# Performance work log

Measured on AMD Instinct MI355X. Metric: run time of the kernel, lower is better.

The kernel has to match this reference:

```python
import jax, jax.numpy as jnp
import numpy as np

B, H, W, CIN, COUT = 4, 128, 128, 16, 16
FH, FW = 2 * H - 1, 2 * W - 1  # fft_shape = 2*k - 1 per spatial dim (SAME, stride 1)


def setup_inputs() -> dict:
    key = jax.random.key(0)
    k1, k2, k3, k4 = jax.random.split(key, 4)
    inputs = jax.random.normal(k1, (B, H, W, CIN), dtype=jnp.float32)
    # Fourier-space complex kernel, represented as two real arrays
    kernel_real = jax.random.normal(k2, (FH, FW, CIN, COUT), dtype=jnp.float32) * 0.05
    kernel_imag = jax.random.normal(k3, (FH, FW, CIN, COUT), dtype=jnp.float32) * 0.05
    bias = jax.random.normal(k4, (1, 1, 1, COUT), dtype=jnp.float32) * 0.01
    return {"inputs": inputs, "kernel_real": kernel_real, "kernel_imag": kernel_imag, "bias": bias}


def reference(inputs, kernel_real, kernel_imag, bias):
    kernel = kernel_real + 1j * kernel_imag  # (FH, FW, CIN, COUT) complex64
    b, h, w, cin = inputs.shape
    fft_shape = (2 * h - 1, 2 * w - 1)
    # FFT over spatial dims, zero-padded to fft_shape -> (B, FH, FW, CIN) complex64
    y = jnp.fft.fftn(inputs, axes=(1, 2), s=fft_shape)
    # Broadcast complex multiply + inverse FFT: (B, FH, FW, CIN, COUT)
    y = jnp.fft.ifftn(y[..., None] * kernel, axes=(1, 2)).real
    # 'SAME' slice: center crop back to the input spatial size
    sh = (fft_shape[0] - h) // 2
    sw = (fft_shape[1] - w) // 2
    y = y[:, sh:sh + h, sw:sw + w]  # (B, H, W, CIN, COUT)
    # Faithful to the source: sum over axis=-1 (the `features` axis), leaving CIN channels
    y = jnp.sum(y, axis=-1)  # (B, H, W, CIN)
    return y + bias  # bias broadcasts because COUT == CIN
```

## Files before the change

kernel.cpp:

```cpp
#include <hip/hip_runtime.h>
#include <math.h>


constexpr float PI2_OVER_N = 6.28318530717958647692f / 255.0f;
constexpr float INV_N2 = 1.0f / (255.0f * 255.0f);

typedef __attribute__((ext_vector_type(8))) short bf16x8;
typedef __attribute__((ext_vector_type(4))) float f32x4;
#define MFMA16 __builtin_amdgcn_mfma_f32_16x16x32_bf16

__device__ __forceinline__ int remap_bc(int xidx) {
  int k = xidx & 7, j = xidx >> 3;
  return ((k >> 1) * 16) + ((k & 1) * 8) + j;
}

__device__ __forceinline__ unsigned short bf16h(float f) {
  unsigned u = __float_as_uint(f);
  return (unsigned short)((u + 0x7FFFu + ((u >> 16) & 1u)) >> 16);
}
__device__ __forceinline__ float bf16f(unsigned short h) {
  return __uint_as_float(((unsigned)h) << 16);
}


__device__ __forceinline__ void ksum_body(
    int buf, int xb, const float* __restrict__ kr, const float* __restrict__ ki,
    float* __restrict__ Sr, float* __restrict__ Si) {
  const int nrows = 255 * 255 * 16;
  int r = xb * 256 + threadIdx.x;
  if (r >= nrows) return;
  const float* src = (buf == 0) ? kr : ki;
  float* dst = (buf == 0) ? Sr : Si;
  const float4* k4 = (const float4*)(src + (size_t)r * 16);
  float4 a = k4[0], b = k4[1], c = k4[2], d = k4[3];
  dst[r] = a.x + a.y + a.z + a.w + b.x + b.y + b.z + b.w +
           c.x + c.y + c.z + c.w + d.x + d.y + d.z + d.w;
}

__device__ __forceinline__ void packx_body(
    int pid, const float* __restrict__ x, short* __restrict__ xp) {
  int bc = pid & 63;
  int mt = pid >> 6;
  int b = bc >> 4, c = bc & 15;
  int mcol = threadIdx.x & 15;
  int noct = threadIdx.x >> 4;
  int m = mt * 16 + mcol;
  const float* xs = x + ((size_t)(b * 128 + m) * 128 + noct * 8) * 16 + c;
  unsigned short hi[8], lo[8];
#pragma unroll
  for (int j = 0; j < 8; ++j) {
    float v = xs[j * 16];
    hi[j] = bf16h(v);
    lo[j] = bf16h(v - bf16f(hi[j]));
  }
  size_t base = (size_t)bc * 32768 + ((size_t)(mt * 16 + noct) * 16 + mcol) * 8;
  uint4 o;
  o.x = (unsigned)hi[0] | ((unsigned)hi[1] << 16);
  o.y = (unsigned)hi[2] | ((unsigned)hi[3] << 16);
  o.z = (unsigned)hi[4] | ((unsigned)hi[5] << 16);
  o.w = (unsigned)hi[6] | ((unsigned)hi[7] << 16);
  *(uint4*)(xp + base) = o;
  o.x = (unsigned)lo[0] | ((unsigned)lo[1] << 16);
  o.y = (unsigned)lo[2] | ((unsigned)lo[3] << 16);
  o.z = (unsigned)lo[4] | ((unsigned)lo[5] << 16);
  o.w = (unsigned)lo[6] | ((unsigned)lo[7] << 16);
  *(uint4*)(xp + base + 16384) = o;
}

__device__ __forceinline__ void buildt1_body(int cid, short* __restrict__ t1) {
  int i = cid * 256 + threadIdx.x;
  int plane = i >> 14;
  int r = i & 16383;
  int qt = r >> 11, noct = (r >> 7) & 15, qcol = (r >> 3) & 15, j = r & 7;
  int q = qt * 16 + qcol, n = noct * 8 + j;
  float s, c;
  sincosf(PI2_OVER_N * (float)((q * n) % 255), &s, &c);
  float src = (plane < 2) ? c : -s;
  unsigned short hh = bf16h(src);
  t1[i] = (short)((plane & 1) ? bf16h(src - bf16f(hh)) : hh);
}

__device__ __forceinline__ void buildt24_body(
    int cid2, short* __restrict__ t2, short* __restrict__ t4, short* __restrict__ t5) {
  int i = cid2 * 256 + threadIdx.x;
  float s, c;
  if (i < 196608) {
    int plane = i >> 15;
    int r = i & 32767;
    int pt = r >> 11, r2 = r & 2047;
    int moct = r2 >> 7, p = (r2 >> 3) & 15, j = r2 & 7;
    int pg = pt * 16 + p, m = moct * 8 + j;
    int k = ((pg % 255) * m) % 255;
    sincosf(PI2_OVER_N * (float)k, &s, &c);
    float ti = -s;
    float src = (plane < 2) ? c : ((plane < 4) ? ti : -ti);
    unsigned short h = bf16h(src);
    t2[i] = (short)((plane & 1) ? bf16h(src - bf16f(h)) : h);
  } else if (i < 393216) {
    int i2 = i - 196608;
    int plane = i2 >> 15;
    int r = i2 & 32767;
    int ht = r >> 12, r2 = r & 4095;
    int poct = r2 >> 7, h = (r2 >> 3) & 15, j = r2 & 7;
    int p = poct * 8 + j;
    unsigned short val = 0;
    if (p < 255) {
      int hg = ht * 16 + h;
      int k = ((hg + 63) * p) % 255;
      sincosf(PI2_OVER_N * (float)k, &s, &c);
      float src = (plane < 2) ? c : ((plane < 4) ? s : -s);
      unsigned short hh = bf16h(src);
      val = (plane & 1) ? bf16h(src - bf16f(hh)) : hh;
    }
    t4[i2] = (short)val;
  } else {
    int i3 = i - 393216;
    int plane = i3 >> 15;
    int r = i3 & 32767;
    int wt = r >> 12, r2 = r & 4095;
    int ko = r2 >> 7, wl = (r2 >> 3) & 15, j = r2 & 7;
    int q = (ko * 8 + j) & 127;
    int ww = wt * 16 + wl;
    sincosf(PI2_OVER_N * (float)(((ww + 63) * q) % 255), &s, &c);
    float src = (plane < 2) ? c : -s;
    unsigned short hh = bf16h(src);
    t5[i3] = (short)((plane & 1) ? bf16h(src - bf16f(hh)) : hh);
  }
}

__global__ __launch_bounds__(256) void fused_front(
    const float* __restrict__ kr, const float* __restrict__ ki,
    float* __restrict__ Sr, float* __restrict__ Si,
    const float* __restrict__ x, short* __restrict__ xp,
    short* __restrict__ t1, short* __restrict__ t2,
    short* __restrict__ t4, short* __restrict__ t5) {
  int bid = blockIdx.x;
  int d = bid >> 2, r = bid & 3;
  if (r == 3) {
    if (d < 512)      packx_body(d, x, xp);
    else if (d < 768) buildt1_body(d - 512, t1);
    else              buildt24_body(d - 768, t2, t4, t5);
  } else {
    int kid = d * 3 + r;
    if (kid < 8192) ksum_body(kid & 1, kid >> 1, kr, ki, Sr, Si);
  }
}


__device__ __forceinline__ void fold_body(
    int fid, const float* __restrict__ Sr, const float* __restrict__ Si,
    float2* __restrict__ keff2) {
  int p = fid % 255;
  int qy = fid / 255;
  int q = qy * 16 + (threadIdx.x >> 4);
  int c = threadIdx.x & 15;
  int pp = (255 - p) % 255;
  int qq = (255 - q) % 255;
  size_t i0 = (size_t)(p * 255 + q) * 16 + c;
  size_t i1 = (size_t)(pp * 255 + qq) * 16 + c;
  float sr0 = Sr[i0], si0 = Si[i0], sr1 = Sr[i1], si1 = Si[i1];
  float2 v;
  v.x = 0.5f * (sr0 + sr1);
  v.y = 0.5f * (si0 - si1);
  keff2[((size_t)c * 255 + p) * 128 + q] = v;
}

__device__ __forceinline__ void s1g_body(
    int gid, const short* __restrict__ xp, const short* __restrict__ t1,
    short* __restrict__ ub) {
  int bc = gid & 63;
  int mt = gid >> 6;
  int w = threadIdx.x >> 6;
  int lane = threadIdx.x & 63;
  int quad = lane >> 4, col = lane & 15;
  f32x4 ur[2] = {{0,0,0,0},{0,0,0,0}};
  f32x4 ui[2] = {{0,0,0,0},{0,0,0,0}};
  const short* xb = xp + (size_t)bc * 32768;
#pragma unroll
  for (int ko = 0; ko < 4; ++ko) {
    int noct = ko * 4 + quad;
    const short* pa = xb + ((size_t)(mt * 16 + noct) * 16 + col) * 8;
    bf16x8 xh = *(const bf16x8*)(pa);
    bf16x8 xl = *(const bf16x8*)(pa + 16384);
#pragma unroll
    for (int qq = 0; qq < 2; ++qq) {
      int qt = w * 2 + qq;
      const short* pb = t1 + ((size_t)(qt * 16 + noct) * 16 + col) * 8;
      bf16x8 ch = *(const bf16x8*)(pb);
      bf16x8 cl = *(const bf16x8*)(pb + 16384);
      bf16x8 nh = *(const bf16x8*)(pb + 2 * 16384);
      bf16x8 nl = *(const bf16x8*)(pb + 3 * 16384);
      ur[qq] = MFMA16(xh, ch, ur[qq], 0, 0, 0);
      ur[qq] = MFMA16(xh, cl, ur[qq], 0, 0, 0);
      ur[qq] = MFMA16(xl, ch, ur[qq], 0, 0, 0);
      ur[qq] = MFMA16(xl, cl, ur[qq], 0, 0, 0);
      ui[qq] = MFMA16(xh, nh, ui[qq], 0, 0, 0);
      ui[qq] = MFMA16(xh, nl, ui[qq], 0, 0, 0);
      ui[qq] = MFMA16(xl, nh, ui[qq], 0, 0, 0);
      ui[qq] = MFMA16(xl, nl, ui[qq], 0, 0, 0);
    }
  }
  int moct = mt * 2 + (quad >> 1);
  int j0 = (quad & 1) * 4;
#pragma unroll
  for (int qq = 0; qq < 2; ++qq) {
    int qt = w * 2 + qq;
    unsigned short rh[4], rl[4], ih[4], il[4];
#pragma unroll
    for (int r = 0; r < 4; ++r) {
      rh[r] = bf16h(ur[qq][r]); rl[r] = bf16h(ur[qq][r] - bf16f(rh[r]));
      ih[r] = bf16h(ui[qq][r]); il[r] = bf16h(ui[qq][r] - bf16f(ih[r]));
    }
    size_t base = (size_t)bc * 65536 + (size_t)qt * 2048 + (size_t)moct * 128 +
                  (size_t)col * 8 + j0;
    uint2 o;
    o.x = (unsigned)rh[0] | ((unsigned)rh[1] << 16);
    o.y = (unsigned)rh[2] | ((unsigned)rh[3] << 16);
    *(uint2*)(ub + base) = o;
    o.x = (unsigned)rl[0] | ((unsigned)rl[1] << 16);
    o.y = (unsigned)rl[2] | ((unsigned)rl[3] << 16);
    *(uint2*)(ub + base + 16384) = o;
    o.x = (unsigned)ih[0] | ((unsigned)ih[1] << 16);
    o.y = (unsigned)ih[2] | ((unsigned)ih[3] << 16);
    *(uint2*)(ub + base + 2 * 16384) = o;
    o.x = (unsigned)il[0] | ((unsigned)il[1] << 16);
    o.y = (unsigned)il[2] | ((unsigned)il[3] << 16);
    *(uint2*)(ub + base + 3 * 16384) = o;
  }
}

__global__ __launch_bounds__(256) void mid(
    const float* __restrict__ Sr, const float* __restrict__ Si,
    float2* __restrict__ keff2,
    const short* __restrict__ xp, const short* __restrict__ t1,
    short* __restrict__ ub) {
  int bid = blockIdx.x;
  int d = bid / 5, r = bid - d * 5;
  if (r == 4) {
    s1g_body(d, xp, t1, ub);
  } else {
    int fid = d * 4 + r;
    if (fid < 2040) fold_body(fid, Sr, Si, keff2);
  }
}

__global__ __launch_bounds__(256) void stage2_mfma(
    const short* __restrict__ ub, const short* __restrict__ t2,
    const float2* __restrict__ keff2, short* __restrict__ zb) {
  int bc = remap_bc(blockIdx.x);
  int c = bc & 15;
  int w = threadIdx.x >> 6;
  int lane = threadIdx.x & 63;
  int quad = lane >> 4, col = lane & 15;
  int pt0 = blockIdx.y * 2;
  int qh = w;
  f32x4 accr[2][2] = {{{0,0,0,0},{0,0,0,0}},{{0,0,0,0},{0,0,0,0}}};
  f32x4 acci[2][2] = {{{0,0,0,0},{0,0,0,0}},{{0,0,0,0},{0,0,0,0}}};
  const short* ubase = ub + (size_t)bc * 65536;
#pragma unroll
  for (int ko = 0; ko < 4; ++ko) {
    int moct = ko * 4 + quad;
    bf16x8 brh[2], brl[2], bih[2], bil[2];
#pragma unroll
    for (int qq = 0; qq < 2; ++qq) {
      int qt = qh * 2 + qq;
      const short* tb = ubase + ((size_t)(qt * 16 + moct) * 16 + col) * 8;
      brh[qq] = *(const bf16x8*)(tb);
      brl[qq] = *(const bf16x8*)(tb + 16384);
      bih[qq] = *(const bf16x8*)(tb + 2 * 16384);
      bil[qq] = *(const bf16x8*)(tb + 3 * 16384);
    }
#pragma unroll
    for (int ptl = 0; ptl < 2; ++ptl) {
      int pt = pt0 + ptl;
      const short* ta = t2 + ((size_t)(pt * 16 + moct) * 16 + col) * 8;
      bf16x8 arh = *(const bf16x8*)(ta);
      bf16x8 arl = *(const bf16x8*)(ta + 32768);
      bf16x8 aih = *(const bf16x8*)(ta + 2 * 32768);
      bf16x8 ail = *(const bf16x8*)(ta + 3 * 32768);
      bf16x8 anh = *(const bf16x8*)(ta + 4 * 32768);
      bf16x8 anl = *(const bf16x8*)(ta + 5 * 32768);
#pragma unroll
      for (int qq = 0; qq < 2; ++qq) {
        accr[ptl][qq] = MFMA16(arh, brh[qq], accr[ptl][qq], 0, 0, 0);
        accr[ptl][qq] = MFMA16(arh, brl[qq], accr[ptl][qq], 0, 0, 0);
        accr[ptl][qq] = MFMA16(arl, brh[qq], accr[ptl][qq], 0, 0, 0);
        accr[ptl][qq] = MFMA16(anh, bih[qq], accr[ptl][qq], 0, 0, 0);
        accr[ptl][qq] = MFMA16(anh, bil[qq], accr[ptl][qq], 0, 0, 0);
        accr[ptl][qq] = MFMA16(anl, bih[qq], accr[ptl][qq], 0, 0, 0);
        acci[ptl][qq] = MFMA16(arh, bih[qq], acci[ptl][qq], 0, 0, 0);
        acci[ptl][qq] = MFMA16(arh, bil[qq], acci[ptl][qq], 0, 0, 0);
        acci[ptl][qq] = MFMA16(arl, bih[qq], acci[ptl][qq], 0, 0, 0);
        acci[ptl][qq] = MFMA16(aih, brh[qq], acci[ptl][qq], 0, 0, 0);
        acci[ptl][qq] = MFMA16(aih, brl[qq], acci[ptl][qq], 0, 0, 0);
        acci[ptl][qq] = MFMA16(ail, brh[qq], acci[ptl][qq], 0, 0, 0);
      }
    }
  }
  size_t joff = (size_t)col * 8 + (quad & 1) * 4;
#pragma unroll
  for (int ptl = 0; ptl < 2; ++ptl) {
    int pt = pt0 + ptl;
    int poct = pt * 2 + (quad >> 1);
#pragma unroll
    for (int qq = 0; qq < 2; ++qq) {
      int qt = qh * 2 + qq;
      int qg = qt * 16 + col;
      float zr[4], zi[4];
#pragma unroll
      for (int r = 0; r < 4; ++r) {
        int pg = pt * 16 + quad * 4 + r;
        int pgc = pg < 255 ? pg : 254;
        float2 k = keff2[((size_t)c * 255 + pgc) * 128 + qg];
        float xr = accr[ptl][qq][r], xi = acci[ptl][qq][r];
        zr[r] = k.x * xr - k.y * xi;
        zi[r] = k.x * xi + k.y * xr;
      }
      unsigned short hr[4], lr[4], hi_[4], li[4];
#pragma unroll
      for (int r = 0; r < 4; ++r) {
        hr[r] = bf16h(zr[r]);  lr[r] = bf16h(zr[r] - bf16f(hr[r]));
        hi_[r] = bf16h(zi[r]); li[r] = bf16h(zi[r] - bf16f(hi_[r]));
      }
      size_t base = (size_t)bc * 131072 + (size_t)qt * 4096 + (size_t)poct * 128 + joff;
      uint2 o;
      o.x = (unsigned)hr[0] | ((unsigned)hr[1] << 16);
      o.y = (unsigned)hr[2] | ((unsigned)hr[3] << 16);
      *(uint2*)(zb + base) = o;
      o.x = (unsigned)lr[0] | ((unsigned)lr[1] << 16);
      o.y = (unsigned)lr[2] | ((unsigned)lr[3] << 16);
      *(uint2*)(zb + base + 32768) = o;
      o.x = (unsigned)hi_[0] | ((unsigned)hi_[1] << 16);
      o.y = (unsigned)hi_[2] | ((unsigned)hi_[3] << 16);
      *(uint2*)(zb + base + 2 * 32768) = o;
      o.x = (unsigned)li[0] | ((unsigned)li[1] << 16);
      o.y = (unsigned)li[2] | ((unsigned)li[3] << 16);
      *(uint2*)(zb + base + 3 * 32768) = o;
    }
  }
}

__global__ __launch_bounds__(256) void stage4_mfma(
    const short* __restrict__ zb, const short* __restrict__ t4,
    short* __restrict__ a5, float* __restrict__ v0) {
  int bc = remap_bc(blockIdx.x);
  int w = threadIdx.x >> 6;
  int lane = threadIdx.x & 63;
  int quad = lane >> 4, col = lane & 15;
  int u = blockIdx.y * 4 + w;
  int qt = u >> 3;
  int kseg = (u >> 2) & 1;
  int htp = u & 3;
  f32x4 accr[2] = {{0,0,0,0},{0,0,0,0}};
  f32x4 acci[2] = {{0,0,0,0},{0,0,0,0}};
  const short* zbase = zb + (size_t)bc * 131072;
#pragma unroll
  for (int ko = 0; ko < 4; ++ko) {
    int poct = kseg * 16 + ko * 4 + quad;
    const short* tz = zbase + ((size_t)(qt * 32 + poct) * 16 + col) * 8;
    bf16x8 zrh = *(const bf16x8*)(tz);
    bf16x8 zrl = *(const bf16x8*)(tz + 32768);
    bf16x8 zih = *(const bf16x8*)(tz + 2 * 32768);
    bf16x8 zil = *(const bf16x8*)(tz + 3 * 32768);
#pragma unroll
    for (int t = 0; t < 2; ++t) {
      int ht = htp * 2 + t;
      const short* ta = t4 + ((size_t)(ht * 32 + poct) * 16 + col) * 8;
      bf16x8 trh = *(const bf16x8*)(ta);
      bf16x8 trl = *(const bf16x8*)(ta + 32768);
      bf16x8 tih = *(const bf16x8*)(ta + 2 * 32768);
      bf16x8 til = *(const bf16x8*)(ta + 3 * 32768);
      bf16x8 tnh = *(const bf16x8*)(ta + 4 * 32768);
      bf16x8 tnl = *(const bf16x8*)(ta + 5 * 32768);
      accr[t] = MFMA16(zrh, trh, accr[t], 0, 0, 0);
      accr[t] = MFMA16(zrh, trl, accr[t], 0, 0, 0);
      accr[t] = MFMA16(zrl, trh, accr[t], 0, 0, 0);
      accr[t] = MFMA16(zih, tnh, accr[t], 0, 0, 0);
      accr[t] = MFMA16(zih, tnl, accr[t], 0, 0, 0);
      accr[t] = MFMA16(zil, tnh, accr[t], 0, 0, 0);
      acci[t] = MFMA16(zih, trh, acci[t], 0, 0, 0);
      acci[t] = MFMA16(zih, trl, acci[t], 0, 0, 0);
      acci[t] = MFMA16(zil, trh, acci[t], 0, 0, 0);
      acci[t] = MFMA16(zrh, tih, acci[t], 0, 0, 0);
      acci[t] = MFMA16(zrh, til, acci[t], 0, 0, 0);
      acci[t] = MFMA16(zrl, tih, acci[t], 0, 0, 0);
    }
  }
  int ko_s = kseg * 16 + qt * 2 + (quad >> 1);
  int j0 = (quad & 1) * 4;
#pragma unroll
  for (int t = 0; t < 2; ++t) {
    int ht = htp * 2 + t;
    unsigned short vh[4], vl[4], wh[4], wl2[4];
#pragma unroll
    for (int r = 0; r < 4; ++r) {
      vh[r] = bf16h(accr[t][r]);  vl[r] = bf16h(accr[t][r] - bf16f(vh[r]));
      wh[r] = bf16h(acci[t][r]);  wl2[r] = bf16h(acci[t][r] - bf16f(wh[r]));
    }
    size_t base = (((size_t)(bc * 4) * 8 + ht) * 32 + ko_s) * 128 + (size_t)col * 8 + j0;
    uint2 o;
    o.x = (unsigned)vh[0] | ((unsigned)vh[1] << 16);
    o.y = (unsigned)vh[2] | ((unsigned)vh[3] << 16);
    *(uint2*)(a5 + base) = o;
    o.x = (unsigned)vl[0] | ((unsigned)vl[1] << 16);
    o.y = (unsigned)vl[2] | ((unsigned)vl[3] << 16);
    *(uint2*)(a5 + base + 32768) = o;
    o.x = (unsigned)wh[0] | ((unsigned)wh[1] << 16);
    o.y = (unsigned)wh[2] | ((unsigned)wh[3] << 16);
    *(uint2*)(a5 + base + 2 * 32768) = o;
    o.x = (unsigned)wl2[0] | ((unsigned)wl2[1] << 16);
    o.y = (unsigned)wl2[2] | ((unsigned)wl2[3] << 16);
    *(uint2*)(a5 + base + 3 * 32768) = o;
    if (qt == 0 && quad == 0)
      v0[(size_t)(kseg * 64 + bc) * 128 + ht * 16 + col] = accr[t][0];
  }
}

__global__ __launch_bounds__(256) void stage5_mfma(
    const short* __restrict__ a5, const short* __restrict__ t5,
    const float* __restrict__ v0, const float* __restrict__ bias,
    float* __restrict__ out) {
  int bc = remap_bc(blockIdx.x);
  int w = threadIdx.x >> 6;
  int lane = threadIdx.x & 63;
  int quad = lane >> 4, col = lane & 15;
  int u = blockIdx.y * 4 + w;
  int ht = u >> 2;
  int wtp = u & 3;
  f32x4 acc[2] = {{0,0,0,0},{0,0,0,0}};
  const short* abase = a5 + (size_t)bc * 131072;
#pragma unroll
  for (int kc = 0; kc < 8; ++kc) {
    int koq = kc * 4 + quad;
    const short* pa = abase + ((size_t)(ht * 32 + koq) * 16 + col) * 8;
    bf16x8 vrh = *(const bf16x8*)(pa);
    bf16x8 vrl = *(const bf16x8*)(pa + 32768);
    bf16x8 vih = *(const bf16x8*)(pa + 2 * 32768);
    bf16x8 vil = *(const bf16x8*)(pa + 3 * 32768);
#pragma unroll
    for (int t = 0; t < 2; ++t) {
      int wt = wtp * 2 + t;
      const short* pb = t5 + ((size_t)(wt * 32 + koq) * 16 + col) * 8;
      bf16x8 tch = *(const bf16x8*)(pb);
      bf16x8 tcl = *(const bf16x8*)(pb + 32768);
      bf16x8 tnh = *(const bf16x8*)(pb + 2 * 32768);
      bf16x8 tnl = *(const bf16x8*)(pb + 3 * 32768);
      acc[t] = MFMA16(vrh, tch, acc[t], 0, 0, 0);
      acc[t] = MFMA16(vrh, tcl, acc[t], 0, 0, 0);
      acc[t] = MFMA16(vrl, tch, acc[t], 0, 0, 0);
      acc[t] = MFMA16(vih, tnh, acc[t], 0, 0, 0);
      acc[t] = MFMA16(vih, tnl, acc[t], 0, 0, 0);
      acc[t] = MFMA16(vil, tnh, acc[t], 0, 0, 0);
    }
  }
  int b = bc >> 4, c = bc & 15;
  float bb = bias[c];
  float v0t[4];
#pragma unroll
  for (int r = 0; r < 4; ++r) {
    int h = ht * 16 + quad * 4 + r;
    v0t[r] = v0[(size_t)bc * 128 + h] + v0[(size_t)(64 + bc) * 128 + h];
  }
#pragma unroll
  for (int t = 0; t < 2; ++t) {
    int ww = (wtp * 2 + t) * 16 + col;
#pragma unroll
    for (int r = 0; r < 4; ++r) {
      int h = ht * 16 + quad * 4 + r;
      out[((size_t)(b * 128 + h) * 128 + ww) * 16 + c] =
          (2.0f * acc[t][r] - v0t[r]) * INV_N2 + bb;
    }
  }
}

extern "C" void kernel_launch(void* const* d_in, const int* in_sizes, int n_in,
                              void* d_out, int out_size, void* d_ws, size_t ws_size,
                              hipStream_t stream) {
  const float* x  = (const float*)d_in[0];
  const float* kr = (const float*)d_in[1];
  const float* ki = (const float*)d_in[2];
  const float* bs = (const float*)d_in[3];
  float* out = (float*)d_out;

  char* p = (char*)d_ws;
  float2* keff2 = (float2*)p; p += (size_t)16 * 255 * 128 * 8;
  short*  zb    = (short*)p;  p += (size_t)64 * 131072 * 2;
  char*   a5reg = p;
  short*  a5    = (short*)p;  p += (size_t)64 * 131072 * 2;
  short*  ub    = (short*)p;  p += (size_t)64 * 65536 * 2;
  short*  t2    = (short*)p;  p += (size_t)196608 * 2;
  short*  t4    = (short*)p;  p += (size_t)196608 * 2;
  short*  t5    = (short*)p;  p += (size_t)131072 * 2;
  float*  v0    = (float*)p;  p += (size_t)2 * 64 * 128 * 4;
  float* Sr = (float*)zb;
  float* Si = Sr + 255 * 255 * 16;
  short* xp = (short*)a5reg;
  short* t1 = (short*)(a5reg + 6 * 1024 * 1024);

  fused_front<<<11264, 256, 0, stream>>>(kr, ki, Sr, Si, x, xp, t1, t2, t4, t5);
  mid<<<2560, 256, 0, stream>>>(Sr, Si, keff2, xp, t1, ub);
  stage2_mfma<<<dim3(64, 8), 256, 0, stream>>>(ub, t2, keff2, zb);
  stage4_mfma<<<dim3(64, 16), 256, 0, stream>>>(zb, t4, a5, v0);
  stage5_mfma<<<dim3(64, 8), 256, 0, stream>>>(a5, t5, v0, bs, out);
}
```

Before: 208.3 us.

## Fuse back-end stages into one persistent kernel with grid barriers

Replaces the four back-end launches (mid, stage2, stage4, stage5) with a single persistent kernel of 512 blocks. The blocks loop over the old work items and use a global atomic-based grid barrier between stages. This removes launch gaps and per-kernel drain/fill overhead. In exchange it needs all 512 blocks to be co-resident (launch_bounds 256,2 on 256 CUs) or the barrier deadlocks, and it adds an extra memset plus the cost of the barrier spin.

```diff
diff --git a/kernel.cpp b/kernel.cpp
--- a/kernel.cpp
+++ b/kernel.cpp
@@ -4,6 +4,7 @@
 
 constexpr float PI2_OVER_N = 6.28318530717958647692f / 255.0f;
 constexpr float INV_N2 = 1.0f / (255.0f * 255.0f);
+constexpr unsigned NBLK = 512;
 
 typedef __attribute__((ext_vector_type(8))) short bf16x8;
 typedef __attribute__((ext_vector_type(4))) float f32x4;
@@ -20,6 +21,23 @@
 }
 __device__ __forceinline__ float bf16f(unsigned short h) {
   return __uint_as_float(((unsigned)h) << 16);
+}
+
+__device__ __forceinline__ void grid_barrier(unsigned* bar, unsigned* gen) {
+  __syncthreads();
+  if (threadIdx.x == 0) {
+    unsigned g = __hip_atomic_load(gen, __ATOMIC_RELAXED, __HIP_MEMORY_SCOPE_AGENT);
+    unsigned a = __hip_atomic_fetch_add(bar, 1u, __ATOMIC_ACQ_REL, __HIP_MEMORY_SCOPE_AGENT);
+    if (a == NBLK - 1) {
+      __hip_atomic_store(bar, 0u, __ATOMIC_RELAXED, __HIP_MEMORY_SCOPE_AGENT);
+      __hip_atomic_store(gen, g + 1u, __ATOMIC_RELEASE, __HIP_MEMORY_SCOPE_AGENT);
+    } else {
+      while (__hip_atomic_load(gen, __ATOMIC_ACQUIRE, __HIP_MEMORY_SCOPE_AGENT) == g) {
+        __builtin_amdgcn_s_sleep(8);
+      }
+    }
+  }
+  __syncthreads();
 }
 
 
@@ -229,30 +247,15 @@
   }
 }
 
-__global__ __launch_bounds__(256) void mid(
-    const float* __restrict__ Sr, const float* __restrict__ Si,
-    float2* __restrict__ keff2,
-    const short* __restrict__ xp, const short* __restrict__ t1,
-    short* __restrict__ ub) {
-  int bid = blockIdx.x;
-  int d = bid / 5, r = bid - d * 5;
-  if (r == 4) {
-    s1g_body(d, xp, t1, ub);
-  } else {
-    int fid = d * 4 + r;
-    if (fid < 2040) fold_body(fid, Sr, Si, keff2);
-  }
-}
-
-__global__ __launch_bounds__(256) void stage2_mfma(
-    const short* __restrict__ ub, const short* __restrict__ t2,
+__device__ __forceinline__ void s2_item(
+    int item, const short* __restrict__ ub, const short* __restrict__ t2,
     const float2* __restrict__ keff2, short* __restrict__ zb) {
-  int bc = remap_bc(blockIdx.x);
+  int bc = remap_bc(item & 63);
   int c = bc & 15;
   int w = threadIdx.x >> 6;
   int lane = threadIdx.x & 63;
   int quad = lane >> 4, col = lane & 15;
-  int pt0 = blockIdx.y * 2;
+  int pt0 = (item >> 6) * 2;
   int qh = w;
   f32x4 accr[2][2] = {{{0,0,0,0},{0,0,0,0}},{{0,0,0,0},{0,0,0,0}}};
   f32x4 acci[2][2] = {{{0,0,0,0},{0,0,0,0}},{{0,0,0,0},{0,0,0,0}}};
@@ -340,14 +343,14 @@
   }
 }
 
-__global__ __launch_bounds__(256) void stage4_mfma(
-    const short* __restrict__ zb, const short* __restrict__ t4,
+__device__ __forceinline__ void s4_item(
+    int item, const short* __restrict__ zb, const short* __restrict__ t4,
     short* __restrict__ a5, float* __restrict__ v0) {
-  int bc = remap_bc(blockIdx.x);
+  int bc = remap_bc(item & 63);
   int w = threadIdx.x >> 6;
   int lane = threadIdx.x & 63;
   int quad = lane >> 4, col = lane & 15;
-  int u = blockIdx.y * 4 + w;
+  int u = (item >> 6) * 4 + w;
   int qt = u >> 3;
   int kseg = (u >> 2) & 1;
   int htp = u & 3;
@@ -416,15 +419,15 @@
   }
 }
 
-__global__ __launch_bounds__(256) void stage5_mfma(
-    const short* __restrict__ a5, const short* __restrict__ t5,
+__device__ __forceinline__ void s5_item(
+    int item, const short* __restrict__ a5, const short* __restrict__ t5,
     const float* __restrict__ v0, const float* __restrict__ bias,
     float* __restrict__ out) {
-  int bc = remap_bc(blockIdx.x);
+  int bc = remap_bc(item & 63);
   int w = threadIdx.x >> 6;
   int lane = threadIdx.x & 63;
   int quad = lane >> 4, col = lane & 15;
-  int u = blockIdx.y * 4 + w;
+  int u = (item >> 6) * 4 + w;
   int ht = u >> 2;
   int wtp = u & 3;
   f32x4 acc[2] = {{0,0,0,0},{0,0,0,0}};
@@ -473,6 +476,31 @@
   }
 }
 
+__global__ __launch_bounds__(256, 2) void backend(
+    const float* Sr, const float* Si, float2* keff2,
+    const short* xp, const short* t1, short* ub,
+    const short* t2, short* zb,
+    const short* t4, short* a5, float* v0,
+    const short* t5, const float* bias, float* out,
+    unsigned* bar, unsigned* gen) {
+  int blk = blockIdx.x;
+  for (int it = blk; it < 2560; it += 512) {
+    int d = it / 5, r = it - d * 5;
+    if (r == 4) {
+      s1g_body(d, xp, t1, ub);
+    } else {
+      int fid = d * 4 + r;
+      if (fid < 2040) fold_body(fid, Sr, Si, keff2);
+    }
+  }
+  grid_barrier(bar, gen);
+  s2_item(blk, ub, t2, keff2, zb);
+  grid_barrier(bar, gen);
+  for (int it = blk; it < 1024; it += 512) s4_item(it, zb, t4, a5, v0);
+  grid_barrier(bar, gen);
+  s5_item(blk, a5, t5, v0, bias, out);
+}
+
 extern "C" void kernel_launch(void* const* d_in, const int* in_sizes, int n_in,
                               void* d_out, int out_size, void* d_ws, size_t ws_size,
                               hipStream_t stream) {
@@ -492,14 +520,14 @@
   short*  t4    = (short*)p;  p += (size_t)196608 * 2;
   short*  t5    = (short*)p;  p += (size_t)131072 * 2;
   float*  v0    = (float*)p;  p += (size_t)2 * 64 * 128 * 4;
+  unsigned* barws = (unsigned*)p; p += 256;
   float* Sr = (float*)zb;
   float* Si = Sr + 255 * 255 * 16;
   short* xp = (short*)a5reg;
   short* t1 = (short*)(a5reg + 6 * 1024 * 1024);
 
+  hipMemsetAsync(barws, 0, 2 * sizeof(unsigned), stream);
   fused_front<<<11264, 256, 0, stream>>>(kr, ki, Sr, Si, x, xp, t1, t2, t4, t5);
-  mid<<<2560, 256, 0, stream>>>(Sr, Si, keff2, xp, t1, ub);
-  stage2_mfma<<<dim3(64, 8), 256, 0, stream>>>(ub, t2, keff2, zb);
-  stage4_mfma<<<dim3(64, 16), 256, 0, stream>>>(zb, t4, a5, v0);
-  stage5_mfma<<<dim3(64, 8), 256, 0, stream>>>(a5, t5, v0, bs, out);
-}
+  backend<<<NBLK, 256, 0, stream>>>(Sr, Si, keff2, xp, t1, ub, t2, zb,
+                                    t4, a5, v0, t5, bs, out, barws, barws + 1);
+}
```

After: 429.8 us. +106.4%, slower.

## Fuse stage4 and stage5 MFMA kernels through shared-memory intermediate

Applied to the files above, without the earlier changes.

Merges the stage4 and stage5 DFT matmul kernels into one kernel. Each block computes one ht row-tile of the stage4 result into LDS (split bf16 hi/lo real and imaginary parts) and then runs the stage5 matmul from LDS, so the a5 and v0 global round trip and one launch go away. In exchange the per-block stage4 tile is computed by 4 waves looping over 4 sub-tiles, with less ILP per wave, and 32KB of LDS per block may limit occupancy.

```diff
diff --git a/kernel.cpp b/kernel.cpp
--- a/kernel.cpp
+++ b/kernel.cpp
@@ -340,31 +340,33 @@
   }
 }
 
-__global__ __launch_bounds__(256) void stage4_mfma(
+__global__ __launch_bounds__(256) void stage45(
     const short* __restrict__ zb, const short* __restrict__ t4,
-    short* __restrict__ a5, float* __restrict__ v0) {
+    const short* __restrict__ t5, const float* __restrict__ bias,
+    float* __restrict__ out) {
+  __shared__ __align__(16) short vlds[4 * 32 * 128];
+  __shared__ float vz[2][16];
   int bc = remap_bc(blockIdx.x);
+  int ht = blockIdx.y;
   int w = threadIdx.x >> 6;
   int lane = threadIdx.x & 63;
   int quad = lane >> 4, col = lane & 15;
-  int u = blockIdx.y * 4 + w;
-  int qt = u >> 3;
-  int kseg = (u >> 2) & 1;
-  int htp = u & 3;
-  f32x4 accr[2] = {{0,0,0,0},{0,0,0,0}};
-  f32x4 acci[2] = {{0,0,0,0},{0,0,0,0}};
   const short* zbase = zb + (size_t)bc * 131072;
 #pragma unroll
-  for (int ko = 0; ko < 4; ++ko) {
-    int poct = kseg * 16 + ko * 4 + quad;
-    const short* tz = zbase + ((size_t)(qt * 32 + poct) * 16 + col) * 8;
-    bf16x8 zrh = *(const bf16x8*)(tz);
-    bf16x8 zrl = *(const bf16x8*)(tz + 32768);
-    bf16x8 zih = *(const bf16x8*)(tz + 2 * 32768);
-    bf16x8 zil = *(const bf16x8*)(tz + 3 * 32768);
-#pragma unroll
-    for (int t = 0; t < 2; ++t) {
-      int ht = htp * 2 + t;
+  for (int i = 0; i < 4; ++i) {
+    int tt = w * 4 + i;
+    int qt = tt >> 1;
+    int kseg = tt & 1;
+    f32x4 accr = {0, 0, 0, 0};
+    f32x4 acci = {0, 0, 0, 0};
+#pragma unroll
+    for (int ko = 0; ko < 4; ++ko) {
+      int poct = kseg * 16 + ko * 4 + quad;
+      const short* tz = zbase + ((size_t)(qt * 32 + poct) * 16 + col) * 8;
+      bf16x8 zrh = *(const bf16x8*)(tz);
+      bf16x8 zrl = *(const bf16x8*)(tz + 32768);
+      bf16x8 zih = *(const bf16x8*)(tz + 2 * 32768);
+      bf16x8 zil = *(const bf16x8*)(tz + 3 * 32768);
       const short* ta = t4 + ((size_t)(ht * 32 + poct) * 16 + col) * 8;
       bf16x8 trh = *(const bf16x8*)(ta);
       bf16x8 trl = *(const bf16x8*)(ta + 32768);
@@ -372,74 +374,57 @@
       bf16x8 til = *(const bf16x8*)(ta + 3 * 32768);
       bf16x8 tnh = *(const bf16x8*)(ta + 4 * 32768);
       bf16x8 tnl = *(const bf16x8*)(ta + 5 * 32768);
-      accr[t] = MFMA16(zrh, trh, accr[t], 0, 0, 0);
-      accr[t] = MFMA16(zrh, trl, accr[t], 0, 0, 0);
-      accr[t] = MFMA16(zrl, trh, accr[t], 0, 0, 0);
-      accr[t] = MFMA16(zih, tnh, accr[t], 0, 0, 0);
-      accr[t] = MFMA16(zih, tnl, accr[t], 0, 0, 0);
-      accr[t] = MFMA16(zil, tnh, accr[t], 0, 0, 0);
-      acci[t] = MFMA16(zih, trh, acci[t], 0, 0, 0);
-      acci[t] = MFMA16(zih, trl, acci[t], 0, 0, 0);
-      acci[t] = MFMA16(zil, trh, acci[t], 0, 0, 0);
-      acci[t] = MFMA16(zrh, tih, acci[t], 0, 0, 0);
-      acci[t] = MFMA16(zrh, til, acci[t], 0, 0, 0);
-      acci[t] = MFMA16(zrl, tih, acci[t], 0, 0, 0);
-    }
-  }
-  int ko_s = kseg * 16 + qt * 2 + (quad >> 1);
-  int j0 = (quad & 1) * 4;
-#pragma unroll
-  for (int t = 0; t < 2; ++t) {
-    int ht = htp * 2 + t;
+      accr = MFMA16(zrh, trh, accr, 0, 0, 0);
+      accr = MFMA16(zrh, trl, accr, 0, 0, 0);
+      accr = MFMA16(zrl, trh, accr, 0, 0, 0);
+      accr = MFMA16(zih, tnh, accr, 0, 0, 0);
+      accr = MFMA16(zih, tnl, accr, 0, 0, 0);
+      accr = MFMA16(zil, tnh, accr, 0, 0, 0);
+      acci = MFMA16(zih, trh, acci, 0, 0, 0);
+      acci = MFMA16(zih, trl, acci, 0, 0, 0);
+      acci = MFMA16(zil, trh, acci, 0, 0, 0);
+      acci = MFMA16(zrh, tih, acci, 0, 0, 0);
+      acci = MFMA16(zrh, til, acci, 0, 0, 0);
+      acci = MFMA16(zrl, tih, acci, 0, 0, 0);
+    }
+    int ko_s = kseg * 16 + qt * 2 + (quad >> 1);
+    int j0 = (quad & 1) * 4;
     unsigned short vh[4], vl[4], wh[4], wl2[4];
 #pragma unroll
     for (int r = 0; r < 4; ++r) {
-      vh[r] = bf16h(accr[t][r]);  vl[r] = bf16h(accr[t][r] - bf16f(vh[r]));
-      wh[r] = bf16h(acci[t][r]);  wl2[r] = bf16h(acci[t][r] - bf16f(wh[r]));
-    }
-    size_t base = (((size_t)(bc * 4) * 8 + ht) * 32 + ko_s) * 128 + (size_t)col * 8 + j0;
+      vh[r] = bf16h(accr[r]);  vl[r] = bf16h(accr[r] - bf16f(vh[r]));
+      wh[r] = bf16h(acci[r]);  wl2[r] = bf16h(acci[r] - bf16f(wh[r]));
+    }
+    short* dst = vlds + (size_t)ko_s * 128 + (size_t)col * 8 + j0;
     uint2 o;
     o.x = (unsigned)vh[0] | ((unsigned)vh[1] << 16);
     o.y = (unsigned)vh[2] | ((unsigned)vh[3] << 16);
-    *(uint2*)(a5 + base) = o;
+    *(uint2*)(dst) = o;
     o.x = (unsigned)vl[0] | ((unsigned)vl[1] << 16);
     o.y = (unsigned)vl[2] | ((unsigned)vl[3] << 16);
-    *(uint2*)(a5 + base + 32768) = o;
+    *(uint2*)(dst + 4096) = o;
     o.x = (unsigned)wh[0] | ((unsigned)wh[1] << 16);
     o.y = (unsigned)wh[2] | ((unsigned)wh[3] << 16);
-    *(uint2*)(a5 + base + 2 * 32768) = o;
+    *(uint2*)(dst + 2 * 4096) = o;
     o.x = (unsigned)wl2[0] | ((unsigned)wl2[1] << 16);
     o.y = (unsigned)wl2[2] | ((unsigned)wl2[3] << 16);
-    *(uint2*)(a5 + base + 3 * 32768) = o;
+    *(uint2*)(dst + 3 * 4096) = o;
     if (qt == 0 && quad == 0)
-      v0[(size_t)(kseg * 64 + bc) * 128 + ht * 16 + col] = accr[t][0];
-  }
-}
-
-__global__ __launch_bounds__(256) void stage5_mfma(
-    const short* __restrict__ a5, const short* __restrict__ t5,
-    const float* __restrict__ v0, const float* __restrict__ bias,
-    float* __restrict__ out) {
-  int bc = remap_bc(blockIdx.x);
-  int w = threadIdx.x >> 6;
-  int lane = threadIdx.x & 63;
-  int quad = lane >> 4, col = lane & 15;
-  int u = blockIdx.y * 4 + w;
-  int ht = u >> 2;
-  int wtp = u & 3;
+      vz[kseg][col] = accr[0];
+  }
+  __syncthreads();
   f32x4 acc[2] = {{0,0,0,0},{0,0,0,0}};
-  const short* abase = a5 + (size_t)bc * 131072;
 #pragma unroll
   for (int kc = 0; kc < 8; ++kc) {
     int koq = kc * 4 + quad;
-    const short* pa = abase + ((size_t)(ht * 32 + koq) * 16 + col) * 8;
+    const short* pa = vlds + (size_t)koq * 128 + (size_t)col * 8;
     bf16x8 vrh = *(const bf16x8*)(pa);
-    bf16x8 vrl = *(const bf16x8*)(pa + 32768);
-    bf16x8 vih = *(const bf16x8*)(pa + 2 * 32768);
-    bf16x8 vil = *(const bf16x8*)(pa + 3 * 32768);
+    bf16x8 vrl = *(const bf16x8*)(pa + 4096);
+    bf16x8 vih = *(const bf16x8*)(pa + 2 * 4096);
+    bf16x8 vil = *(const bf16x8*)(pa + 3 * 4096);
 #pragma unroll
     for (int t = 0; t < 2; ++t) {
-      int wt = wtp * 2 + t;
+      int wt = w * 2 + t;
       const short* pb = t5 + ((size_t)(wt * 32 + koq) * 16 + col) * 8;
       bf16x8 tch = *(const bf16x8*)(pb);
       bf16x8 tcl = *(const bf16x8*)(pb + 32768);
@@ -457,13 +442,11 @@
   float bb = bias[c];
   float v0t[4];
 #pragma unroll
-  for (int r = 0; r < 4; ++r) {
-    int h = ht * 16 + quad * 4 + r;
-    v0t[r] = v0[(size_t)bc * 128 + h] + v0[(size_t)(64 + bc) * 128 + h];
-  }
+  for (int r = 0; r < 4; ++r)
+    v0t[r] = vz[0][quad * 4 + r] + vz[1][quad * 4 + r];
 #pragma unroll
   for (int t = 0; t < 2; ++t) {
-    int ww = (wtp * 2 + t) * 16 + col;
+    int ww = (w * 2 + t) * 16 + col;
 #pragma unroll
     for (int r = 0; r < 4; ++r) {
       int h = ht * 16 + quad * 4 + r;
@@ -485,21 +468,18 @@
   char* p = (char*)d_ws;
   float2* keff2 = (float2*)p; p += (size_t)16 * 255 * 128 * 8;
   short*  zb    = (short*)p;  p += (size_t)64 * 131072 * 2;
-  char*   a5reg = p;
-  short*  a5    = (short*)p;  p += (size_t)64 * 131072 * 2;
+  char*   scr   = p;          p += (size_t)64 * 131072 * 2;
   short*  ub    = (short*)p;  p += (size_t)64 * 65536 * 2;
   short*  t2    = (short*)p;  p += (size_t)196608 * 2;
   short*  t4    = (short*)p;  p += (size_t)196608 * 2;
   short*  t5    = (short*)p;  p += (size_t)131072 * 2;
-  float*  v0    = (float*)p;  p += (size_t)2 * 64 * 128 * 4;
   float* Sr = (float*)zb;
   float* Si = Sr + 255 * 255 * 16;
-  short* xp = (short*)a5reg;
-  short* t1 = (short*)(a5reg + 6 * 1024 * 1024);
+  short* xp = (short*)scr;
+  short* t1 = (short*)(scr + 6 * 1024 * 1024);
 
   fused_front<<<11264, 256, 0, stream>>>(kr, ki, Sr, Si, x, xp, t1, t2, t4, t5);
   mid<<<2560, 256, 0, stream>>>(Sr, Si, keff2, xp, t1, ub);
   stage2_mfma<<<dim3(64, 8), 256, 0, stream>>>(ub, t2, keff2, zb);
-  stage4_mfma<<<dim3(64, 16), 256, 0, stream>>>(zb, t4, a5, v0);
-  stage5_mfma<<<dim3(64, 8), 256, 0, stream>>>(a5, t5, v0, bs, out);
-}
+  stage45<<<dim3(64, 8), 256, 0, stream>>>(zb, t4, t5, bs, out);
+}
```

Result: faster. 203.8 us (-2.1%).
